# Optimization experiments

Hardware: AMD Instinct MI355X
Metric: run time of the kernel (lower is better)

Reference implementation:

```python
import jax, jax.numpy as jnp
import numpy as np

B, TOK, D, H, L = 64, 20, 512, 8, 4
S = 512          # tokens per half
HD = D // H
ODIM = 32        # encoder_output_dim


def _ln(x, g, b):
    m = x.mean(-1, keepdims=True)
    v = ((x - m) ** 2).mean(-1, keepdims=True)
    return (x - m) / jnp.sqrt(v + 1e-5) * g + b


def _alibi_slopes(h):
    # mirrors FlashAttentionBlock.build_alibi_slopes (base=2.0)
    base = 2.0
    return jnp.asarray([1.0 / base ** (i // (h // base)) for i in range(h)], dtype=jnp.float32)


def setup_inputs() -> dict:
    key = jax.random.key(0)
    ks = jax.random.split(key, 16)
    r = lambda i, shape, s=0.02: jax.random.normal(ks[i], shape, jnp.float32) * s
    return {
        'x': jax.random.normal(ks[0], (B, 2 * S * TOK), jnp.float32),
        'in_W': r(1, (TOK, D)), 'in_b': jnp.zeros((D,)),
        'qkv_W': r(2, (L, D, 3 * D)), 'qkv_b': jnp.zeros((L, 3 * D)),
        'ln1_g': jnp.ones((L, D)), 'ln1_b': jnp.zeros((L, D)),
        'ffn_W1': r(3, (L, D, 4 * D)), 'ffn_b1': jnp.zeros((L, 4 * D)),
        'ffn_W2': r(4, (L, 4 * D, D)), 'ffn_b2': jnp.zeros((L, D)),
        'ln2_g': jnp.ones((L, D)), 'ln2_b': jnp.zeros((L, D)),
        'out_W': r(5, (D, ODIM)), 'out_b': jnp.zeros((ODIM,)),
        'd1_W': r(6, (2 * S * ODIM, 256)), 'd1_b': jnp.zeros((256,)),
        'bn1_g': jnp.ones((256,)), 'bn1_b': jnp.zeros((256,)),
        'bn1_m': jnp.zeros((256,)), 'bn1_v': jnp.ones((256,)),
        'd2_W': r(7, (256, 128)), 'd2_b': jnp.zeros((128,)),
        'bn2_g': jnp.ones((128,)), 'bn2_b': jnp.zeros((128,)),
        'bn2_m': jnp.zeros((128,)), 'bn2_v': jnp.ones((128,)),
        'fin_W': r(8, (128, 1)), 'fin_b': jnp.zeros((1,)),
    }


def _forward(x, in_W, in_b, qkv_W, qkv_b, ln1_g, ln1_b, ffn_W1, ffn_b1,
             ffn_W2, ffn_b2, ln2_g, ln2_b, out_W, out_b,
             d1_W, d1_b, bn1_g, bn1_b, bn1_m, bn1_v,
             d2_W, d2_b, bn2_g, bn2_b, bn2_m, bn2_v, fin_W, fin_b):
    slopes = _alibi_slopes(H)                                   # [H]
    pos = jnp.arange(S)
    # non-causal ALiBi bias: -slope * |i - j|, shape [H, S, S]
    bias = -slopes[:, None, None] * jnp.abs(pos[:, None] - pos[None, :]).astype(jnp.float32)
    scale = 1.0 / np.sqrt(HD).astype(np.float32)

    def encode(xh):
        b = xh.shape[0]
        t = xh.reshape(b, S, TOK) @ in_W + in_b                 # [b, S, D]
        for l in range(L):
            res = t
            qkv = (t @ qkv_W[l] + qkv_b[l]).reshape(b, S, 3, H, HD)
            q, k, v = qkv[:, :, 0], qkv[:, :, 1], qkv[:, :, 2]  # [b, S, H, HD]
            scores = jnp.einsum('bqhd,bkhd->bhqk', q, k) * scale + bias[None]
            attn = jax.nn.softmax(scores, axis=-1)
            o = jnp.einsum('bhqk,bkhd->bqhd', attn, v).reshape(b, S, D)
            t = _ln(res + o, ln1_g[l], ln1_b[l])
            res = t
            f = jax.nn.relu(t @ ffn_W1[l] + ffn_b1[l]) @ ffn_W2[l] + ffn_b2[l]
            t = _ln(res + f, ln2_g[l], ln2_b[l])
        return (t @ out_W + out_b).reshape(b, -1)               # [b, S*ODIM]

    half = S * TOK
    h = jnp.concatenate([encode(x[:, :half]), encode(x[:, half:])], axis=-1)
    bn = lambda z, g, bb, m, v: (z - m) / jnp.sqrt(v + 1e-5) * g + bb
    h = bn(jax.nn.relu(h @ d1_W + d1_b), bn1_g, bn1_b, bn1_m, bn1_v)
    h = bn(jax.nn.relu(h @ d2_W + d2_b), bn2_g, bn2_b, bn2_m, bn2_v)
    return (h @ fin_W + fin_b).squeeze(-1)                      # [B]


def reference(x, in_W, in_b, qkv_W, qkv_b, ln1_g, ln1_b, ffn_W1, ffn_b1,
              ffn_W2, ffn_b2, ln2_g, ln2_b, out_W, out_b,
              d1_W, d1_b, bn1_g, bn1_b, bn1_m, bn1_v,
              d2_W, d2_b, bn2_g, bn2_b, bn2_m, bn2_v, fin_W, fin_b):
    return _forward(x, in_W, in_b, qkv_W, qkv_b, ln1_g, ln1_b, ffn_W1, ffn_b1,
                    ffn_W2, ffn_b2, ln2_g, ln2_b, out_W, out_b,
                    d1_W, d1_b, bn1_g, bn1_b, bn1_m, bn1_v,
                    d2_W, d2_b, bn2_g, bn2_b, bn2_m, bn2_v, fin_W, fin_b)
```

## Files before the change

kernel.cpp:

```cpp
#include <hip/hip_runtime.h>

#define DEV __device__ __forceinline__

using bf16x8 = __attribute__((ext_vector_type(8))) __bf16;
using f32x4  = __attribute__((ext_vector_type(4))) float;
using u16x8  = __attribute__((ext_vector_type(8))) unsigned short;
using u16x4  = __attribute__((ext_vector_type(4))) unsigned short;

DEV unsigned short f2bf(float f) {
  unsigned u = __builtin_bit_cast(unsigned, f);
  u += 0x7fffu + ((u >> 16) & 1u);
  return (unsigned short)(u >> 16);
}
DEV float bf2f(unsigned short h) {
  unsigned u = ((unsigned)h) << 16;
  return __builtin_bit_cast(float, u);
}
DEV f32x4 mfma16(u16x8 a, u16x8 b, f32x4 c) {
  return __builtin_amdgcn_mfma_f32_16x16x32_bf16(
      __builtin_bit_cast(bf16x8, a), __builtin_bit_cast(bf16x8, b), c, 0, 0, 0);
}
DEV f32x4 zero4() { f32x4 z = {0.f, 0.f, 0.f, 0.f}; return z; }

DEV void glds16(const unsigned short* g, unsigned short* l) {
  __builtin_amdgcn_global_load_lds(
      (const __attribute__((address_space(1))) unsigned int*)g,
      (__attribute__((address_space(3))) unsigned int*)l, 16, 0, 0);
}

#define PH_BAR()                          \
  do {                                    \
    __builtin_amdgcn_sched_barrier(0);    \
    __builtin_amdgcn_s_barrier();         \
    __builtin_amdgcn_sched_barrier(0);    \
  } while (0)

enum { EPI_BIAS = 0, EPI_RELU = 1, EPI_OUT = 2 };

template <int EPI>
__global__ __launch_bounds__(512, 1) void gemm8p_k(
    const unsigned short* __restrict__ A, const unsigned short* __restrict__ Bt,
    const float* __restrict__ bias, unsigned short* __restrict__ C, int N, int K) {
  __shared__ unsigned short As[2][16384];
  __shared__ unsigned short Bs[2][16384];
  const int tid = threadIdx.x;
  const int lane = tid & 63, wv = tid >> 6;
  const int q = lane >> 4, ln = lane & 15;
  const int wr = wv >> 2, wc = wv & 3;
  const int ln7 = ln & 7;

  const int Nt = gridDim.x, Mt = gridDim.y;
  const int lin = blockIdx.x + Nt * blockIdx.y;
  const int xcd = lin & 7;
  const int j = lin >> 3;
  const int mi = xcd * (Mt >> 3) + j / Nt;
  const int ni = j % Nt;
  const int m0 = mi << 8, n0 = ni << 8;

  f32x4 acc[8][4];
#pragma unroll
  for (int i = 0; i < 8; ++i)
#pragma unroll
    for (int jj = 0; jj < 4; ++jj) acc[i][jj] = zero4();

  const int sr = lane >> 3;
  const int sc = ((lane & 7) ^ sr) << 3;
  const unsigned short* Abase = A + (size_t)(m0 + wv * 8 + sr) * K + sc;
  const unsigned short* Bbase = Bt + (size_t)(n0 + wv * 8 + sr) * K + sc;

  const int T = K >> 6;

  auto stA = [&](int buf, int t, int half) {
    unsigned short* d = &As[buf][(half * 128 + wv * 8) * 64];
    const unsigned short* s = Abase + (size_t)(half * 128) * K + t * 64;
    glds16(s, d);
    glds16(s + (size_t)64 * K, d + 4096);
  };
  auto stB = [&](int buf, int t, int half) {
    unsigned short* d = &Bs[buf][(half * 128 + wv * 8) * 64];
    const unsigned short* s = Bbase + (size_t)(half * 128) * K + t * 64;
    glds16(s, d);
    glds16(s + (size_t)64 * K, d + 4096);
  };

  stB(0, 0, 0);
  stB(0, 0, 1);
  stA(0, 0, 0);
  stA(0, 0, 1);
  if (T > 1) {
    stB(1, 1, 0);
    stB(1, 1, 1);
    asm volatile("s_waitcnt vmcnt(4)" ::: "memory");
  } else {
    asm volatile("s_waitcnt vmcnt(0)" ::: "memory");
  }
  PH_BAR();

  for (int u = 0; u < T; ++u) {
    const int cur = u & 1, nxt = cur ^ 1;
    const unsigned short* Ab = &As[cur][0];
    const unsigned short* Bb = &Bs[cur][0];
    u16x8 a0[4][2], a1[4][2], b0[2][2], b1[2][2];

#pragma unroll
    for (int mt = 0; mt < 4; ++mt)
#pragma unroll
      for (int kk = 0; kk < 2; ++kk)
        a0[mt][kk] = *(const u16x8*)(Ab + (wr * 128 + mt * 16 + ln) * 64 +
                                     (((kk * 4 + q) ^ ln7) << 3));
#pragma unroll
    for (int nt = 0; nt < 2; ++nt)
#pragma unroll
      for (int kk = 0; kk < 2; ++kk)
        b0[nt][kk] = *(const u16x8*)(Bb + (wc * 64 + nt * 16 + ln) * 64 +
                                     (((kk * 4 + q) ^ ln7) << 3));
    if (u + 1 < T) stA(nxt, u + 1, 0);
    PH_BAR();
    __builtin_amdgcn_s_setprio(1);
#pragma unroll
    for (int kk = 0; kk < 2; ++kk)
#pragma unroll
      for (int nt = 0; nt < 2; ++nt)
#pragma unroll
        for (int mt = 0; mt < 4; ++mt)
          acc[mt][nt] = mfma16(a0[mt][kk], b0[nt][kk], acc[mt][nt]);
    __builtin_amdgcn_s_setprio(0);
    PH_BAR();

#pragma unroll
    for (int nt = 0; nt < 2; ++nt)
#pragma unroll
      for (int kk = 0; kk < 2; ++kk)
        b1[nt][kk] = *(const u16x8*)(Bb + (wc * 64 + (nt + 2) * 16 + ln) * 64 +
                                     (((kk * 4 + q) ^ ln7) << 3));
    if (u + 1 < T) stA(nxt, u + 1, 1);
    PH_BAR();
    __builtin_amdgcn_s_setprio(1);
#pragma unroll
    for (int kk = 0; kk < 2; ++kk)
#pragma unroll
      for (int nt = 0; nt < 2; ++nt)
#pragma unroll
        for (int mt = 0; mt < 4; ++mt)
          acc[mt][nt + 2] = mfma16(a0[mt][kk], b1[nt][kk], acc[mt][nt + 2]);
    __builtin_amdgcn_s_setprio(0);
    PH_BAR();

#pragma unroll
    for (int mt = 0; mt < 4; ++mt)
#pragma unroll
      for (int kk = 0; kk < 2; ++kk)
        a1[mt][kk] = *(const u16x8*)(Ab + (wr * 128 + (mt + 4) * 16 + ln) * 64 +
                                     (((kk * 4 + q) ^ ln7) << 3));
    if (u + 2 < T) stB(cur, u + 2, 0);
    PH_BAR();
    __builtin_amdgcn_s_setprio(1);
#pragma unroll
    for (int kk = 0; kk < 2; ++kk)
#pragma unroll
      for (int nt = 0; nt < 2; ++nt)
#pragma unroll
        for (int mt = 0; mt < 4; ++mt)
          acc[mt + 4][nt] = mfma16(a1[mt][kk], b0[nt][kk], acc[mt + 4][nt]);
    __builtin_amdgcn_s_setprio(0);
    PH_BAR();

    if (u + 2 < T) stB(cur, u + 2, 1);
    PH_BAR();
    __builtin_amdgcn_s_setprio(1);
#pragma unroll
    for (int kk = 0; kk < 2; ++kk)
#pragma unroll
      for (int nt = 0; nt < 2; ++nt)
#pragma unroll
        for (int mt = 0; mt < 4; ++mt)
          acc[mt + 4][nt + 2] = mfma16(a1[mt][kk], b1[nt][kk], acc[mt + 4][nt + 2]);
    __builtin_amdgcn_s_setprio(0);
    if (u + 1 < T) {
      if (u + 2 < T) {
        asm volatile("s_waitcnt vmcnt(4)" ::: "memory");
      } else {
        asm volatile("s_waitcnt vmcnt(0)" ::: "memory");
      }
      PH_BAR();
    }
  }

#pragma unroll
  for (int mt = 0; mt < 8; ++mt) {
    const int rowb = m0 + wr * 128 + mt * 16 + q * 4;
#pragma unroll
    for (int nt = 0; nt < 4; ++nt) {
      const int col = n0 + wc * 64 + nt * 16 + ln;
      const float bs = bias[col];
#pragma unroll
      for (int r = 0; r < 4; ++r) {
        float v = acc[mt][nt][r] + bs;
        if (EPI == EPI_RELU) v = fmaxf(v, 0.f);
        C[(size_t)(rowb + r) * N + col] = f2bf(v);
      }
    }
  }
}

template <int EPI>
__global__ __launch_bounds__(256) void gemm_k(
    const unsigned short* __restrict__ A, const unsigned short* __restrict__ Bt,
    const float* __restrict__ bias, unsigned short* __restrict__ C, int N, int K) {
  __shared__ unsigned short As[128 * 64];
  __shared__ unsigned short Bs[128 * 64];
  const int tid = threadIdx.x;
  const int lane = tid & 63, wv = tid >> 6;
  const int q = lane >> 4, ln = lane & 15;
  const int wr = wv >> 1, wc = wv & 1;

  const int Nt = gridDim.x, Mt = gridDim.y;
  const int lin = blockIdx.x + Nt * blockIdx.y;
  const int xcd = lin & 7;
  const int j = lin >> 3;
  const int mi = xcd * (Mt >> 3) + j / Nt;
  const int ni = j % Nt;
  const int m0 = mi << 7, n0 = ni << 7;

  f32x4 acc[4][4];
#pragma unroll
  for (int i = 0; i < 4; ++i)
#pragma unroll
    for (int jj = 0; jj < 4; ++jj) acc[i][jj] = zero4();

  const int ra = lane >> 3;
  const int ca = ((lane & 7) ^ ra) << 3;
  const unsigned short* Ap = A + (size_t)(m0 + wv * 32 + ra) * K + ca;
  const unsigned short* Bp = Bt + (size_t)(n0 + wv * 32 + ra) * K + ca;
  unsigned short* AsW = As + wv * 2048;
  unsigned short* BsW = Bs + wv * 2048;
  const int ln7 = ln & 7;

  for (int kb = 0; kb < K; kb += 64) {
    __syncthreads();
#pragma unroll
    for (int t = 0; t < 4; ++t) {
      glds16(Ap + (size_t)(t * 8) * K + kb, AsW + t * 512);
      glds16(Bp + (size_t)(t * 8) * K + kb, BsW + t * 512);
    }
    __syncthreads();
#pragma unroll
    for (int kk = 0; kk < 2; ++kk) {
      const int c = kk * 4 + q;
      const int lo = ln * 64 + ((c ^ ln7) << 3);
      u16x8 af[4];
#pragma unroll
      for (int mt = 0; mt < 4; ++mt)
        af[mt] = *(const u16x8*)(As + (wr * 64 + mt * 16) * 64 + lo);
#pragma unroll
      for (int nt = 0; nt < 4; ++nt) {
        u16x8 bf = *(const u16x8*)(Bs + (wc * 64 + nt * 16) * 64 + lo);
#pragma unroll
        for (int mt = 0; mt < 4; ++mt) acc[mt][nt] = mfma16(af[mt], bf, acc[mt][nt]);
      }
    }
  }

#pragma unroll
  for (int mt = 0; mt < 4; ++mt) {
    const int rowb = m0 + wr * 64 + mt * 16 + q * 4;
#pragma unroll
    for (int nt = 0; nt < 4; ++nt) {
      const int col = n0 + wc * 64 + nt * 16 + ln;
      if (EPI == EPI_OUT && col >= 32) continue;
      const float bs = bias[col];
      const int ldc = (EPI == EPI_OUT) ? 32 : N;
#pragma unroll
      for (int r = 0; r < 4; ++r) {
        float v = acc[mt][nt][r] + bs;
        if (EPI == EPI_RELU) v = fmaxf(v, 0.f);
        C[(size_t)(rowb + r) * ldc + col] = f2bf(v);
      }
    }
  }
}

__global__ __launch_bounds__(256) void vt_k(const unsigned short* __restrict__ big,
                                            unsigned short* __restrict__ vt) {
  __shared__ unsigned short td[64 * 72];
  const int tid = threadIdx.x;
  const int sh = blockIdx.x;
  const int seq = sh >> 3, h = sh & 7;
  const int kt = blockIdx.y;
  {
    const int key = tid >> 2, hdc = (tid & 3) << 4;
    const unsigned short* src =
        big + ((size_t)seq * 512 + kt * 64 + key) * 1536 + 1024 + h * 64 + hdc;
    *(u16x8*)(td + key * 72 + hdc) = *(const u16x8*)src;
    *(u16x8*)(td + key * 72 + hdc + 8) = *(const u16x8*)(src + 8);
  }
  __syncthreads();
  {
    const int hd = tid >> 2, kc = (tid & 3) << 4;
    u16x8 a, b;
#pragma unroll
    for (int j = 0; j < 8; ++j) a[j] = td[(kc + j) * 72 + hd];
#pragma unroll
    for (int j = 0; j < 8; ++j) b[j] = td[(kc + 8 + j) * 72 + hd];
    unsigned short* dst = vt + ((size_t)sh * 64 + hd) * 512 + kt * 64 + kc;
    *(u16x8*)dst = a;
    *(u16x8*)(dst + 8) = b;
  }
}

__global__ __launch_bounds__(256) void attn_k(const unsigned short* __restrict__ qkv,
                                              const unsigned short* __restrict__ vt,
                                              unsigned short* __restrict__ o) {
  __shared__ unsigned short Qs[128 * 72];
  __shared__ unsigned short Ks[64 * 64];
  __shared__ unsigned short Vts[64 * 64];
  unsigned short* Ps = Qs;
  const int tid = threadIdx.x;
  const int lane = tid & 63, w = tid >> 6, q = lane >> 4, ln = lane & 15;
  const int bh = blockIdx.x;
  const int seq = bh >> 3, h = bh & 7;
  const int qt = blockIdx.y;
  const size_t tokb = (size_t)seq * 512;
  const int qoff = h * 64, koff = 512 + h * 64;
  const float c1 = 0.125f * 1.44269504f;
  const float c2 = ((h < 4) ? 1.0f : 0.5f) * 1.44269504f;

#pragma unroll
  for (int p = 0; p < 4; ++p) {
    int c = p * 256 + tid;
    int row = c >> 3, cc = (c & 7) << 3;
    u16x8 v = *(const u16x8*)(qkv + (tokb + qt * 128 + row) * 1536 + qoff + cc);
    *(u16x8*)(Qs + row * 72 + cc) = v;
  }
  __syncthreads();
  u16x8 aq[2][2];
#pragma unroll
  for (int mt = 0; mt < 2; ++mt)
#pragma unroll
    for (int kc = 0; kc < 2; ++kc)
      aq[mt][kc] = *(const u16x8*)(Qs + (w * 32 + mt * 16 + ln) * 72 + kc * 32 + q * 8);

  float lacc[2] = {0.f, 0.f};
  f32x4 o_acc[2][4];
#pragma unroll
  for (int mt = 0; mt < 2; ++mt)
#pragma unroll
    for (int ht = 0; ht < 4; ++ht) o_acc[mt][ht] = zero4();

  const int sr = lane >> 3;
  const int sc = ((lane & 7) ^ sr) << 3;
  const unsigned short* Kp = qkv + (tokb + w * 16 + sr) * 1536 + koff + sc;
  const unsigned short* Vp = vt + ((size_t)bh * 64 + w * 16 + sr) * 512 + sc;
  unsigned short* KsW = Ks + w * 1024;
  unsigned short* VsW = Vts + w * 1024;
  const int ln7 = ln & 7;

  for (int kt = 0; kt < 8; ++kt) {
    __syncthreads();
    glds16(Kp + (size_t)(kt * 64) * 1536, KsW);
    glds16(Kp + (size_t)(kt * 64 + 8) * 1536, KsW + 512);
    glds16(Vp + kt * 64, VsW);
    glds16(Vp + kt * 64 + (size_t)8 * 512, VsW + 512);
    __syncthreads();

    f32x4 sacc[2][4];
#pragma unroll
    for (int mt = 0; mt < 2; ++mt)
#pragma unroll
      for (int nt = 0; nt < 4; ++nt) sacc[mt][nt] = zero4();
#pragma unroll
    for (int nt = 0; nt < 4; ++nt)
#pragma unroll
      for (int kc = 0; kc < 2; ++kc) {
        u16x8 bk = *(const u16x8*)(Ks + (nt * 16 + ln) * 64 + (((kc * 4 + q) ^ ln7) << 3));
#pragma unroll
        for (int mt = 0; mt < 2; ++mt) sacc[mt][nt] = mfma16(bk, aq[mt][kc], sacc[mt][nt]);
      }

    const float qp0 = (float)(qt * 128 + w * 32 + ln);
    const float kb0 = (float)(kt * 64 + q * 4);
#pragma unroll
    for (int mt = 0; mt < 2; ++mt) {
      const float qpm = qp0 + (float)(mt * 16);
#pragma unroll
      for (int nt = 0; nt < 4; ++nt) {
        const float kp = kb0 + (float)(nt * 16);
        u16x4 pk;
#pragma unroll
        for (int r = 0; r < 4; ++r) {
          const float ad = fabsf(qpm - (kp + (float)r));
          const float p = exp2f(fmaf(sacc[mt][nt][r], c1, -c2 * ad));
          const unsigned u = __builtin_bit_cast(unsigned, p);
          const unsigned short pb = (unsigned short)((u + 0x8000u) >> 16);
          pk[r] = pb;
          lacc[mt] += bf2f(pb);
        }
        *(u16x4*)(Ps + (w * 32 + mt * 16 + ln) * 72 + nt * 16 + q * 4) = pk;
      }
    }
#pragma unroll
    for (int kc = 0; kc < 2; ++kc) {
      u16x8 pa[2];
#pragma unroll
      for (int mt = 0; mt < 2; ++mt)
        pa[mt] = *(const u16x8*)(Ps + (w * 32 + mt * 16 + ln) * 72 + kc * 32 + q * 8);
#pragma unroll
      for (int ht = 0; ht < 4; ++ht) {
        u16x8 bv = *(const u16x8*)(Vts + (ht * 16 + ln) * 64 + (((kc * 4 + q) ^ ln7) << 3));
#pragma unroll
        for (int mt = 0; mt < 2; ++mt) o_acc[mt][ht] = mfma16(pa[mt], bv, o_acc[mt][ht]);
      }
    }
  }

  float rl[2][4];
#pragma unroll
  for (int mt = 0; mt < 2; ++mt) {
    float l = lacc[mt];
    l += __shfl_xor(l, 16, 64);
    l += __shfl_xor(l, 32, 64);
    const int sb = (lane >> 4) * 20;
#pragma unroll
    for (int r = 0; r < 4; ++r) rl[mt][r] = 1.0f / __shfl(l, sb + r, 64);
  }

#pragma unroll
  for (int mt = 0; mt < 2; ++mt)
#pragma unroll
    for (int ht = 0; ht < 4; ++ht)
#pragma unroll
      for (int r = 0; r < 4; ++r) {
        const int row = qt * 128 + w * 32 + mt * 16 + q * 4 + r;
        const float val = o_acc[mt][ht][r] * rl[mt][r];
        o[(tokb + row) * 512 + h * 64 + ht * 16 + ln] = f2bf(val);
      }
}

__global__ __launch_bounds__(256) void ln_k(const unsigned short* res,
                                            const unsigned short* __restrict__ y,
                                            const float* __restrict__ g,
                                            const float* __restrict__ b,
                                            unsigned short* out) {
  const int lane = threadIdx.x & 63, wv = threadIdx.x >> 6;
  const size_t row = (size_t)blockIdx.x * 4 + wv;
  const size_t base = row * 512 + lane * 8;
  u16x8 rv = *(const u16x8*)(res + base);
  u16x8 yv = *(const u16x8*)(y + base);
  float v[8];
  float s = 0.f, s2 = 0.f;
#pragma unroll
  for (int i = 0; i < 8; ++i) {
    v[i] = bf2f(rv[i]) + bf2f(yv[i]);
    s += v[i];
    s2 += v[i] * v[i];
  }
#pragma unroll
  for (int m = 1; m < 64; m <<= 1) {
    s += __shfl_xor(s, m, 64);
    s2 += __shfl_xor(s2, m, 64);
  }
  const float mean = s * (1.f / 512.f);
  const float var = s2 * (1.f / 512.f) - mean * mean;
  const float rstd = rsqrtf(var + 1e-5f);
  const int c = lane * 8;
  u16x8 ov;
#pragma unroll
  for (int i = 0; i < 8; ++i) ov[i] = f2bf((v[i] - mean) * rstd * g[c + i] + b[c + i]);
  *(u16x8*)(out + base) = ov;
}

__global__ __launch_bounds__(256) void transpose_w(const float* __restrict__ in,
                                                   unsigned short* __restrict__ out,
                                                   int Kin, int Nin, int Kout, int Nout) {
  __shared__ float tile[32][33];
  const int nb = blockIdx.x * 32, kb = blockIdx.y * 32;
  const int tx = threadIdx.x & 31, ty = threadIdx.x >> 5;
#pragma unroll
  for (int i = 0; i < 32; i += 8) {
    int k = kb + ty + i, n = nb + tx;
    tile[ty + i][tx] = (k < Kin && n < Nin) ? in[(size_t)k * Nin + n] : 0.f;
  }
  __syncthreads();
#pragma unroll
  for (int i = 0; i < 32; i += 8) {
    int n = nb + ty + i, k = kb + tx;
    if (n < Nout && k < Kout) out[(size_t)n * Kout + k] = f2bf(tile[tx][ty + i]);
  }
}

__global__ __launch_bounds__(256) void xpad_k(const float* __restrict__ x,
                                              unsigned short* __restrict__ xp) {
  const int idx = blockIdx.x * 256 + threadIdx.x;
  const int tok = idx >> 6, k = idx & 63;
  const int seq = tok >> 9, s = tok & 511;
  const int hf = seq >> 6, b = seq & 63;
  float v = 0.f;
  if (k < 20) v = x[(size_t)b * 20480 + hf * 10240 + s * 20 + k];
  xp[idx] = f2bf(v);
}

__global__ __launch_bounds__(256) void d1_part(const unsigned short* __restrict__ enc,
                                               const float* __restrict__ W,
                                               float* __restrict__ pz) {
  __shared__ float ef[64 * 128];
  const int tid = threadIdx.x;
  const int kb = blockIdx.x * 128;
  const int hf = kb >> 14;
  const int j0 = kb & 16383;
  {
    const int m = tid >> 2, c = (tid & 3) * 32;
    const unsigned short* src = enc + (size_t)hf * 1048576 + (size_t)m * 16384 + j0 + c;
#pragma unroll
    for (int i = 0; i < 4; ++i) {
      u16x8 v = *(const u16x8*)(src + i * 8);
#pragma unroll
      for (int jj = 0; jj < 8; ++jj) ef[m * 128 + c + i * 8 + jj] = bf2f(v[jj]);
    }
  }
  __syncthreads();
  const int n = tid;
  float acc[64];
#pragma unroll
  for (int m = 0; m < 64; ++m) acc[m] = 0.f;
  for (int kc = 0; kc < 128; kc += 4) {
    const float w0 = W[(size_t)(kb + kc) * 256 + n];
    const float w1 = W[(size_t)(kb + kc + 1) * 256 + n];
    const float w2 = W[(size_t)(kb + kc + 2) * 256 + n];
    const float w3 = W[(size_t)(kb + kc + 3) * 256 + n];
#pragma unroll
    for (int m = 0; m < 64; ++m) {
      const f32x4 e = *(const f32x4*)(ef + m * 128 + kc);
      acc[m] += e[0] * w0 + e[1] * w1 + e[2] * w2 + e[3] * w3;
    }
  }
#pragma unroll
  for (int m = 0; m < 64; ++m)
    pz[(size_t)(blockIdx.x * 64 + m) * 256 + n] = acc[m];
}

__global__ __launch_bounds__(256) void d1_fin(const float* __restrict__ pz,
                                              const float* __restrict__ d1b,
                                              const float* __restrict__ g,
                                              const float* __restrict__ b,
                                              const float* __restrict__ mm,
                                              const float* __restrict__ vv,
                                              float* __restrict__ h1) {
  const int m = blockIdx.x, n = threadIdx.x;
  float a = d1b[n];
  for (int sl = 0; sl < 256; ++sl) a += pz[(size_t)(sl * 64 + m) * 256 + n];
  a = fmaxf(a, 0.f);
  a = (a - mm[n]) * rsqrtf(vv[n] + 1e-5f) * g[n] + b[n];
  h1[m * 256 + n] = a;
}

__global__ __launch_bounds__(128) void d2_k(const float* __restrict__ h1,
                                            const float* __restrict__ W,
                                            const float* __restrict__ bb,
                                            const float* __restrict__ g,
                                            const float* __restrict__ b,
                                            const float* __restrict__ mm,
                                            const float* __restrict__ vv,
                                            float* __restrict__ h2) {
  __shared__ float hs[256];
  const int m = blockIdx.x, n = threadIdx.x;
  hs[n] = h1[m * 256 + n];
  hs[n + 128] = h1[m * 256 + n + 128];
  __syncthreads();
  float a = bb[n];
#pragma unroll 8
  for (int k = 0; k < 256; ++k) a += hs[k] * W[k * 128 + n];
  a = fmaxf(a, 0.f);
  a = (a - mm[n]) * rsqrtf(vv[n] + 1e-5f) * g[n] + b[n];
  h2[m * 128 + n] = a;
}

__global__ __launch_bounds__(64) void fin_k(const float* __restrict__ h2,
                                            const float* __restrict__ W,
                                            const float* __restrict__ fb,
                                            float* __restrict__ out) {
  const int m = threadIdx.x;
  float a = fb[0];
#pragma unroll 8
  for (int k = 0; k < 128; ++k) a += h2[m * 128 + k] * W[k];
  out[m] = a;
}

extern "C" void kernel_launch(void* const* d_in, const int* in_sizes, int n_in,
                              void* d_out, int out_size, void* d_ws, size_t ws_size,
                              hipStream_t stream) {
  const float* x      = (const float*)d_in[0];
  const float* in_W   = (const float*)d_in[1];
  const float* in_b   = (const float*)d_in[2];
  const float* qkv_W  = (const float*)d_in[3];
  const float* qkv_b  = (const float*)d_in[4];
  const float* ln1_g  = (const float*)d_in[5];
  const float* ln1_b  = (const float*)d_in[6];
  const float* ffn_W1 = (const float*)d_in[7];
  const float* ffn_b1 = (const float*)d_in[8];
  const float* ffn_W2 = (const float*)d_in[9];
  const float* ffn_b2 = (const float*)d_in[10];
  const float* ln2_g  = (const float*)d_in[11];
  const float* ln2_b  = (const float*)d_in[12];
  const float* out_W  = (const float*)d_in[13];
  const float* out_b  = (const float*)d_in[14];
  const float* d1W    = (const float*)d_in[15];
  const float* d1b    = (const float*)d_in[16];
  const float* bn1g   = (const float*)d_in[17];
  const float* bn1b   = (const float*)d_in[18];
  const float* bn1m   = (const float*)d_in[19];
  const float* bn1v   = (const float*)d_in[20];
  const float* d2W    = (const float*)d_in[21];
  const float* d2b    = (const float*)d_in[22];
  const float* bn2g   = (const float*)d_in[23];
  const float* bn2b   = (const float*)d_in[24];
  const float* bn2m   = (const float*)d_in[25];
  const float* bn2v   = (const float*)d_in[26];
  const float* finW   = (const float*)d_in[27];
  const float* finb   = (const float*)d_in[28];
  (void)in_sizes; (void)n_in; (void)out_size; (void)ws_size;

  char* ws = (char*)d_ws;
  size_t off = 0;
  auto alloc = [&](size_t bytes) {
    char* p = ws + off;
    off += (bytes + 255) & ~(size_t)255;
    return p;
  };
  unsigned short* t     = (unsigned short*)alloc(32768ull * 512 * 2);
  unsigned short* big   = (unsigned short*)alloc(32768ull * 2048 * 2);
  unsigned short* ob    = (unsigned short*)alloc(32768ull * 512 * 2);
  unsigned short* xpad  = (unsigned short*)alloc(65536ull * 64 * 2);
  unsigned short* enc   = (unsigned short*)alloc(65536ull * 32 * 2);
  unsigned short* inWt  = (unsigned short*)alloc(512ull * 64 * 2);
  unsigned short* qkvWt = (unsigned short*)alloc(4ull * 1536 * 512 * 2);
  unsigned short* f1Wt  = (unsigned short*)alloc(4ull * 2048 * 512 * 2);
  unsigned short* f2Wt  = (unsigned short*)alloc(4ull * 512 * 2048 * 2);
  unsigned short* outWt = (unsigned short*)alloc(128ull * 512 * 2);
  float* h1 = (float*)alloc(64ull * 256 * 4);
  float* h2 = (float*)alloc(64ull * 128 * 4);
  float* pz = (float*)big;
  unsigned short* vtb = big + (size_t)32768 * 1536;

  xpad_k<<<16384, 256, 0, stream>>>(x, xpad);
  transpose_w<<<dim3(16, 2), 256, 0, stream>>>(in_W, inWt, 20, 512, 64, 512);
  transpose_w<<<dim3(4, 16), 256, 0, stream>>>(out_W, outWt, 512, 32, 512, 128);
  for (int l = 0; l < 4; ++l) {
    transpose_w<<<dim3(48, 16), 256, 0, stream>>>(qkv_W + (size_t)l * 512 * 1536,
                                                  qkvWt + (size_t)l * 1536 * 512, 512, 1536, 512, 1536);
    transpose_w<<<dim3(64, 16), 256, 0, stream>>>(ffn_W1 + (size_t)l * 512 * 2048,
                                                  f1Wt + (size_t)l * 2048 * 512, 512, 2048, 512, 2048);
    transpose_w<<<dim3(16, 64), 256, 0, stream>>>(ffn_W2 + (size_t)l * 2048 * 512,
                                                  f2Wt + (size_t)l * 512 * 2048, 2048, 512, 2048, 512);
  }

  for (int hf = 0; hf < 2; ++hf) {
    gemm8p_k<EPI_BIAS><<<dim3(2, 128), 512, 0, stream>>>(xpad + (size_t)hf * 32768 * 64, inWt, in_b, t, 512, 64);
    for (int l = 0; l < 4; ++l) {
      gemm8p_k<EPI_BIAS><<<dim3(6, 128), 512, 0, stream>>>(t, qkvWt + (size_t)l * 1536 * 512,
                                                           qkv_b + l * 1536, big, 1536, 512);
      vt_k<<<dim3(512, 8), 256, 0, stream>>>(big, vtb);
      attn_k<<<dim3(512, 4), 256, 0, stream>>>(big, vtb, ob);
      ln_k<<<8192, 256, 0, stream>>>(t, ob, ln1_g + l * 512, ln1_b + l * 512, t);
      gemm8p_k<EPI_RELU><<<dim3(8, 128), 512, 0, stream>>>(t, f1Wt + (size_t)l * 2048 * 512,
                                                           ffn_b1 + l * 2048, big, 2048, 512);
      gemm8p_k<EPI_BIAS><<<dim3(2, 128), 512, 0, stream>>>(big, f2Wt + (size_t)l * 512 * 2048,
                                                           ffn_b2 + l * 512, ob, 512, 2048);
      ln_k<<<8192, 256, 0, stream>>>(t, ob, ln2_g + l * 512, ln2_b + l * 512, t);
    }
    gemm_k<EPI_OUT><<<dim3(1, 256), 256, 0, stream>>>(t, outWt, out_b,
                                                      enc + (size_t)hf * 32768 * 32, 128, 512);
  }

  d1_part<<<256, 256, 0, stream>>>(enc, d1W, pz);
  d1_fin<<<64, 256, 0, stream>>>(pz, d1b, bn1g, bn1b, bn1m, bn1v, h1);
  d2_k<<<64, 128, 0, stream>>>(h1, d2W, d2b, bn2g, bn2b, bn2m, bn2v, h2);
  fin_k<<<1, 64, 0, stream>>>(h2, finW, finb, (float*)d_out);
}
```

Measured before the change: 2.998 ms.

## Fuse V transpose into QKV GEMM epilogue and double-buffer attention K/V tiles

The QKV projection GEMM now writes the V columns straight into a per-head transposed layout from its epilogue, so the separate vt_k transpose kernel and its extra read and write pass over V are gone. The attention kernel double-buffers its K and V shared-memory tiles and prefetches the next key tile while computing the current one, to hide global-load latency. The costs are more LDS per attention block, which may lower occupancy, and narrower scattered 8-byte stores for V in the GEMM epilogue.

```diff
diff --git a/kernel.cpp b/kernel.cpp
--- a/kernel.cpp
+++ b/kernel.cpp
@@ -35,12 +35,13 @@
     __builtin_amdgcn_sched_barrier(0);    \
   } while (0)
 
-enum { EPI_BIAS = 0, EPI_RELU = 1, EPI_OUT = 2 };
+enum { EPI_BIAS = 0, EPI_RELU = 1, EPI_OUT = 2, EPI_QKV = 3 };
 
 template <int EPI>
 __global__ __launch_bounds__(512, 1) void gemm8p_k(
     const unsigned short* __restrict__ A, const unsigned short* __restrict__ Bt,
-    const float* __restrict__ bias, unsigned short* __restrict__ C, int N, int K) {
+    const float* __restrict__ bias, unsigned short* __restrict__ C,
+    unsigned short* __restrict__ Cv, int N, int K) {
   __shared__ unsigned short As[2][16384];
   __shared__ unsigned short Bs[2][16384];
   const int tid = threadIdx.x;
@@ -189,15 +190,24 @@
 #pragma unroll
   for (int mt = 0; mt < 8; ++mt) {
     const int rowb = m0 + wr * 128 + mt * 16 + q * 4;
+    const int seq = rowb >> 9, key0 = rowb & 511;
 #pragma unroll
     for (int nt = 0; nt < 4; ++nt) {
       const int col = n0 + wc * 64 + nt * 16 + ln;
       const float bs = bias[col];
-#pragma unroll
-      for (int r = 0; r < 4; ++r) {
-        float v = acc[mt][nt][r] + bs;
-        if (EPI == EPI_RELU) v = fmaxf(v, 0.f);
-        C[(size_t)(rowb + r) * N + col] = f2bf(v);
+      if (EPI == EPI_QKV && n0 >= 1024) {
+        const int hh = (col - 1024) >> 6, hd = col & 63;
+        u16x4 pk;
+#pragma unroll
+        for (int r = 0; r < 4; ++r) pk[r] = f2bf(acc[mt][nt][r] + bs);
+        *(u16x4*)(Cv + ((size_t)((seq * 8 + hh) * 64 + hd)) * 512 + key0) = pk;
+      } else {
+#pragma unroll
+        for (int r = 0; r < 4; ++r) {
+          float v = acc[mt][nt][r] + bs;
+          if (EPI == EPI_RELU) v = fmaxf(v, 0.f);
+          C[(size_t)(rowb + r) * N + col] = f2bf(v);
+        }
       }
     }
   }
@@ -280,40 +290,12 @@
   }
 }
 
-__global__ __launch_bounds__(256) void vt_k(const unsigned short* __restrict__ big,
-                                            unsigned short* __restrict__ vt) {
-  __shared__ unsigned short td[64 * 72];
-  const int tid = threadIdx.x;
-  const int sh = blockIdx.x;
-  const int seq = sh >> 3, h = sh & 7;
-  const int kt = blockIdx.y;
-  {
-    const int key = tid >> 2, hdc = (tid & 3) << 4;
-    const unsigned short* src =
-        big + ((size_t)seq * 512 + kt * 64 + key) * 1536 + 1024 + h * 64 + hdc;
-    *(u16x8*)(td + key * 72 + hdc) = *(const u16x8*)src;
-    *(u16x8*)(td + key * 72 + hdc + 8) = *(const u16x8*)(src + 8);
-  }
-  __syncthreads();
-  {
-    const int hd = tid >> 2, kc = (tid & 3) << 4;
-    u16x8 a, b;
-#pragma unroll
-    for (int j = 0; j < 8; ++j) a[j] = td[(kc + j) * 72 + hd];
-#pragma unroll
-    for (int j = 0; j < 8; ++j) b[j] = td[(kc + 8 + j) * 72 + hd];
-    unsigned short* dst = vt + ((size_t)sh * 64 + hd) * 512 + kt * 64 + kc;
-    *(u16x8*)dst = a;
-    *(u16x8*)(dst + 8) = b;
-  }
-}
-
 __global__ __launch_bounds__(256) void attn_k(const unsigned short* __restrict__ qkv,
                                               const unsigned short* __restrict__ vt,
                                               unsigned short* __restrict__ o) {
   __shared__ unsigned short Qs[128 * 72];
-  __shared__ unsigned short Ks[64 * 64];
-  __shared__ unsigned short Vts[64 * 64];
+  __shared__ unsigned short Ks[2][64 * 64];
+  __shared__ unsigned short Vts[2][64 * 64];
   unsigned short* Ps = Qs;
   const int tid = threadIdx.x;
   const int lane = tid & 63, w = tid >> 6, q = lane >> 4, ln = lane & 15;
@@ -332,36 +314,51 @@
     u16x8 v = *(const u16x8*)(qkv + (tokb + qt * 128 + row) * 1536 + qoff + cc);
     *(u16x8*)(Qs + row * 72 + cc) = v;
   }
-  __syncthreads();
-  u16x8 aq[2][2];
-#pragma unroll
-  for (int mt = 0; mt < 2; ++mt)
-#pragma unroll
-    for (int kc = 0; kc < 2; ++kc)
-      aq[mt][kc] = *(const u16x8*)(Qs + (w * 32 + mt * 16 + ln) * 72 + kc * 32 + q * 8);
-
-  float lacc[2] = {0.f, 0.f};
-  f32x4 o_acc[2][4];
-#pragma unroll
-  for (int mt = 0; mt < 2; ++mt)
-#pragma unroll
-    for (int ht = 0; ht < 4; ++ht) o_acc[mt][ht] = zero4();
 
   const int sr = lane >> 3;
   const int sc = ((lane & 7) ^ sr) << 3;
   const unsigned short* Kp = qkv + (tokb + w * 16 + sr) * 1536 + koff + sc;
   const unsigned short* Vp = vt + ((size_t)bh * 64 + w * 16 + sr) * 512 + sc;
-  unsigned short* KsW = Ks + w * 1024;
-  unsigned short* VsW = Vts + w * 1024;
   const int ln7 = ln & 7;
 
-  for (int kt = 0; kt < 8; ++kt) {
-    __syncthreads();
+  auto stage = [&](int kt, int buf) {
+    unsigned short* KsW = &Ks[buf][w * 1024];
+    unsigned short* VsW = &Vts[buf][w * 1024];
     glds16(Kp + (size_t)(kt * 64) * 1536, KsW);
     glds16(Kp + (size_t)(kt * 64 + 8) * 1536, KsW + 512);
     glds16(Vp + kt * 64, VsW);
     glds16(Vp + kt * 64 + (size_t)8 * 512, VsW + 512);
+  };
+
+  stage(0, 0);
+
+  __syncthreads();
+  u16x8 aq[2][2];
+#pragma unroll
+  for (int mt = 0; mt < 2; ++mt)
+#pragma unroll
+    for (int kc = 0; kc < 2; ++kc)
+      aq[mt][kc] = *(const u16x8*)(Qs + (w * 32 + mt * 16 + ln) * 72 + kc * 32 + q * 8);
+
+  float lacc[2] = {0.f, 0.f};
+  f32x4 o_acc[2][4];
+#pragma unroll
+  for (int mt = 0; mt < 2; ++mt)
+#pragma unroll
+    for (int ht = 0; ht < 4; ++ht) o_acc[mt][ht] = zero4();
+
+  for (int kt = 0; kt < 8; ++kt) {
+    const int buf = kt & 1;
     __syncthreads();
+    if (kt + 1 < 8) {
+      stage(kt + 1, buf ^ 1);
+      asm volatile("s_waitcnt vmcnt(4)" ::: "memory");
+    } else {
+      asm volatile("s_waitcnt vmcnt(0)" ::: "memory");
+    }
+    __builtin_amdgcn_sched_barrier(0);
+    __builtin_amdgcn_s_barrier();
+    __builtin_amdgcn_sched_barrier(0);
 
     f32x4 sacc[2][4];
 #pragma unroll
@@ -372,7 +369,7 @@
     for (int nt = 0; nt < 4; ++nt)
 #pragma unroll
       for (int kc = 0; kc < 2; ++kc) {
-        u16x8 bk = *(const u16x8*)(Ks + (nt * 16 + ln) * 64 + (((kc * 4 + q) ^ ln7) << 3));
+        u16x8 bk = *(const u16x8*)(&Ks[buf][(nt * 16 + ln) * 64 + (((kc * 4 + q) ^ ln7) << 3)]);
 #pragma unroll
         for (int mt = 0; mt < 2; ++mt) sacc[mt][nt] = mfma16(bk, aq[mt][kc], sacc[mt][nt]);
       }
@@ -406,7 +403,7 @@
         pa[mt] = *(const u16x8*)(Ps + (w * 32 + mt * 16 + ln) * 72 + kc * 32 + q * 8);
 #pragma unroll
       for (int ht = 0; ht < 4; ++ht) {
-        u16x8 bv = *(const u16x8*)(Vts + (ht * 16 + ln) * 64 + (((kc * 4 + q) ^ ln7) << 3));
+        u16x8 bv = *(const u16x8*)(&Vts[buf][(ht * 16 + ln) * 64 + (((kc * 4 + q) ^ ln7) << 3)]);
 #pragma unroll
         for (int mt = 0; mt < 2; ++mt) o_acc[mt][ht] = mfma16(pa[mt], bv, o_acc[mt][ht]);
       }
@@ -654,17 +651,16 @@
   }
 
   for (int hf = 0; hf < 2; ++hf) {
-    gemm8p_k<EPI_BIAS><<<dim3(2, 128), 512, 0, stream>>>(xpad + (size_t)hf * 32768 * 64, inWt, in_b, t, 512, 64);
+    gemm8p_k<EPI_BIAS><<<dim3(2, 128), 512, 0, stream>>>(xpad + (size_t)hf * 32768 * 64, inWt, in_b, t, nullptr, 512, 64);
     for (int l = 0; l < 4; ++l) {
-      gemm8p_k<EPI_BIAS><<<dim3(6, 128), 512, 0, stream>>>(t, qkvWt + (size_t)l * 1536 * 512,
-                                                           qkv_b + l * 1536, big, 1536, 512);
-      vt_k<<<dim3(512, 8), 256, 0, stream>>>(big, vtb);
+      gemm8p_k<EPI_QKV><<<dim3(6, 128), 512, 0, stream>>>(t, qkvWt + (size_t)l * 1536 * 512,
+                                                          qkv_b + l * 1536, big, vtb, 1536, 512);
       attn_k<<<dim3(512, 4), 256, 0, stream>>>(big, vtb, ob);
       ln_k<<<8192, 256, 0, stream>>>(t, ob, ln1_g + l * 512, ln1_b + l * 512, t);
       gemm8p_k<EPI_RELU><<<dim3(8, 128), 512, 0, stream>>>(t, f1Wt + (size_t)l * 2048 * 512,
-                                                           ffn_b1 + l * 2048, big, 2048, 512);
+                                                           ffn_b1 + l * 2048, big, nullptr, 2048, 512);
       gemm8p_k<EPI_BIAS><<<dim3(2, 128), 512, 0, stream>>>(big, f2Wt + (size_t)l * 512 * 2048,
-                                                           ffn_b2 + l * 512, ob, 512, 2048);
+                                                           ffn_b2 + l * 512, ob, nullptr, 512, 2048);
       ln_k<<<8192, 256, 0, stream>>>(t, ob, ln2_g + l * 512, ln2_b + l * 512, t);
     }
     gemm_k<EPI_OUT><<<dim3(1, 256), 256, 0, stream>>>(t, outWt, out_b,
```

Measured after the change: 3.002 ms. About the same (+0.1%).
